# Optimization experiments

Hardware: AMD Instinct MI355X
Metric: run time of the kernel (lower is better)

## Reference

```python
import jax, jax.numpy as jnp
import numpy as np

E = 768   # embed_size
H = 64    # head_embed_size
B = 8
T = 4096  # == ctx_size


def setup_inputs() -> dict:
    key = jax.random.key(0)
    k1, k2, k3, k4 = jax.random.split(key, 4)
    inputs = jax.random.normal(k1, (B, T, E), dtype=jnp.float32)
    # Linear weights stored as (E, H) so projection is x @ W
    scale = 1.0 / np.sqrt(E)
    Wq = jax.random.uniform(k2, (E, H), dtype=jnp.float32, minval=-scale, maxval=scale)
    Wk = jax.random.uniform(k3, (E, H), dtype=jnp.float32, minval=-scale, maxval=scale)
    Wv = jax.random.uniform(k4, (E, H), dtype=jnp.float32, minval=-scale, maxval=scale)
    return {"inputs": inputs, "Wq": Wq, "Wk": Wk, "Wv": Wv}


def reference(inputs, Wq, Wk, Wv):
    Tlen = inputs.shape[1]
    q = inputs @ Wq  # (B,T,H)
    k = inputs @ Wk  # (B,T,H)
    v = inputs @ Wv  # (B,T,H)
    # NOTE: original module does NOT scale by 1/sqrt(H) — faithful reproduction.
    scores = jnp.einsum('bqh,bkh->bqk', q, k)  # (B,T,T)
    causal = jnp.tril(jnp.ones((Tlen, Tlen), dtype=bool))
    scores = jnp.where(causal, scores, -jnp.inf)
    attn = jax.nn.softmax(scores, axis=-1)
    # dropout=0 -> identity
    out = jnp.einsum('bqk,bkh->bqh', attn, v)  # (B,T,H)
    return out
```

## Files before the change

### kernel.cpp

```cpp
#include <hip/hip_runtime.h>
#include <hip/hip_bf16.h>

#define E_DIM 768
#define H_DIM 64
#define B_SZ 8
#define T_SZ 4096
#define BT (B_SZ * T_SZ)

typedef __attribute__((ext_vector_type(8))) short short8;
typedef __attribute__((ext_vector_type(4))) float floatx4;

#define RAWBAR() __asm__ volatile("s_waitcnt lgkmcnt(0)\n\ts_barrier" ::: "memory")

static __device__ __forceinline__ unsigned short bf1(float a) {
    __hip_bfloat16 h = __float2bfloat16(a);
    unsigned short u; __builtin_memcpy(&u, &h, 2); return u;
}
static __device__ __forceinline__ unsigned int pk2(float a, float b) {
    __hip_bfloat162 h = __float22bfloat162_rn(float2{a, b});
    unsigned int u; __builtin_memcpy(&u, &h, 4); return u;
}

__global__ __launch_bounds__(256) void prep_w(
    const float* __restrict__ Wq, const float* __restrict__ Wk,
    const float* __restrict__ Wv, unsigned short* __restrict__ Wt)
{
    __shared__ float Ls[64][65];
    const int nt = blockIdx.x;
    const int kc = blockIdx.y;
    const float* __restrict__ W = (nt == 0) ? Wq : (nt == 1) ? Wk : Wv;
    const float scl = (nt == 0) ? 1.44269504088896f : 1.0f;
    const int t = threadIdx.x;
    const int k0 = kc * 64;

#pragma unroll
    for (int it = 0; it < 16; ++it) {
        const int kk = (t >> 6) + it * 4;
        Ls[kk][t & 63] = W[(size_t)(k0 + kk) * H_DIM + (t & 63)];
    }
    __syncthreads();

#pragma unroll
    for (int it = 0; it < 4; ++it) {
        const int nl = (t >> 4) + it * 16;
        const int kl = (t & 15) * 4;
        unsigned int u[2];
        u[0] = pk2(Ls[kl + 0][nl] * scl, Ls[kl + 1][nl] * scl);
        u[1] = pk2(Ls[kl + 2][nl] * scl, Ls[kl + 3][nl] * scl);
        *(uint2*)(Wt + (size_t)(nt * 64 + nl) * E_DIM + k0 + kl) = *(uint2*)u;
    }
}

__global__ __launch_bounds__(768) void proj_mfma(
    const float* __restrict__ X, const unsigned short* __restrict__ Wt,
    unsigned short* __restrict__ Qb, unsigned short* __restrict__ Kb,
    unsigned short* __restrict__ Vtb)
{
    __shared__ unsigned short Xs[2][16][776];

    const int tid  = threadIdx.x;
    const int wave = tid >> 6, lane = tid & 63;
    const int row  = lane & 15, quad = lane >> 4;
    const int m0   = blockIdx.x * 128;

    short8 bfr[24];
    {
        const unsigned short* wp = Wt + (size_t)(wave * 16 + row) * E_DIM + quad * 8;
#pragma unroll
        for (int ks = 0; ks < 24; ++ks) bfr[ks] = *(const short8*)(wp + ks * 32);
    }

    const int srow = tid & 15;
    const int sc   = tid >> 4;
    const float* __restrict__ xbase = X + (size_t)(m0 + srow) * E_DIM + sc * 16;

    float4 fx[4];
#define LDX(mt)                                                               \
    {                                                                         \
        const float* p = xbase + (size_t)(mt) * 16 * E_DIM;                   \
        fx[0] = *(const float4*)(p);     fx[1] = *(const float4*)(p + 4);     \
        fx[2] = *(const float4*)(p + 8); fx[3] = *(const float4*)(p + 12);    \
    }
#define STX(buf)                                                              \
    {                                                                         \
        unsigned int tmp[8];                                                  \
        tmp[0] = pk2(fx[0].x, fx[0].y); tmp[1] = pk2(fx[0].z, fx[0].w);       \
        tmp[2] = pk2(fx[1].x, fx[1].y); tmp[3] = pk2(fx[1].z, fx[1].w);       \
        tmp[4] = pk2(fx[2].x, fx[2].y); tmp[5] = pk2(fx[2].z, fx[2].w);       \
        tmp[6] = pk2(fx[3].x, fx[3].y); tmp[7] = pk2(fx[3].z, fx[3].w);       \
        *(int4*)&Xs[buf][srow][sc * 16]     = *(int4*)&tmp[0];                \
        *(int4*)&Xs[buf][srow][sc * 16 + 8] = *(int4*)&tmp[4];                \
    }

    LDX(0); STX(0);
    RAWBAR();

    const int g  = wave >> 2;
    const int h  = (wave & 3) * 16 + row;
    unsigned short* __restrict__ OQK = (g == 0) ? Qb : Kb;
    const int bb = m0 >> 12;

    int cur = 0;
    for (int mt = 0; mt < 8; ++mt) {
        if (mt < 7) LDX(mt + 1);

        floatx4 a0 = (floatx4)0.0f, a1 = (floatx4)0.0f;
        floatx4 a2 = (floatx4)0.0f, a3 = (floatx4)0.0f;
#pragma unroll
        for (int ks = 0; ks < 6; ++ks) {
            const short8 f0 = *(const short8*)&Xs[cur][row][(ks * 4 + 0) * 32 + quad * 8];
            const short8 f1 = *(const short8*)&Xs[cur][row][(ks * 4 + 1) * 32 + quad * 8];
            const short8 f2 = *(const short8*)&Xs[cur][row][(ks * 4 + 2) * 32 + quad * 8];
            const short8 f3 = *(const short8*)&Xs[cur][row][(ks * 4 + 3) * 32 + quad * 8];
            a0 = __builtin_amdgcn_mfma_f32_16x16x32_bf16(f0, bfr[ks * 4 + 0], a0, 0, 0, 0);
            a1 = __builtin_amdgcn_mfma_f32_16x16x32_bf16(f1, bfr[ks * 4 + 1], a1, 0, 0, 0);
            a2 = __builtin_amdgcn_mfma_f32_16x16x32_bf16(f2, bfr[ks * 4 + 2], a2, 0, 0, 0);
            a3 = __builtin_amdgcn_mfma_f32_16x16x32_bf16(f3, bfr[ks * 4 + 3], a3, 0, 0, 0);
        }
        floatx4 acc;
#pragma unroll
        for (int r = 0; r < 4; ++r) acc[r] = (a0[r] + a1[r]) + (a2[r] + a3[r]);

        const int mr = m0 + mt * 16 + quad * 4;
        if (g < 2) {
#pragma unroll
            for (int r = 0; r < 4; ++r)
                OQK[(size_t)(mr + r) * H_DIM + h] = bf1(acc[r]);
        } else {
            const int t0 = mr & 4095;
            unsigned int u[2];
            u[0] = pk2(acc[0], acc[1]); u[1] = pk2(acc[2], acc[3]);
            *(uint2*)(Vtb + ((size_t)bb * H_DIM + h) * T_SZ + t0) = *(uint2*)u;
        }

        if (mt < 7) STX(cur ^ 1);
        RAWBAR();
        cur ^= 1;
    }
#undef LDX
#undef STX
}

__global__ __launch_bounds__(256, 3) void attn_mfma(
    const unsigned short* __restrict__ Qb,
    const unsigned short* __restrict__ Kb,
    const unsigned short* __restrict__ Vtb,
    float* __restrict__ Opart, float* __restrict__ lpart,
    float* __restrict__ Out)
{
    __shared__ __align__(16) unsigned short KVb[2][2][64][72];
    __shared__ __align__(16) unsigned short Ps[4][16][40];
    __shared__ float lc[4][16];

    const int lb   = blockIdx.x;
    const int b    = lb & 7;
    const int s    = lb >> 3;
    const bool split = (s < 128);
    const int qq   = split ? (127 - (s >> 1)) : (191 - s);
    const int half = s & 1;
    const int nkt_tot = (qq >> 1) + 1;
    const int hsp  = (nkt_tot + 1) >> 1;
    const int k0t  = (split && half) ? hsp : 0;
    const int k1t  = (split && !half) ? hsp : nkt_tot;
    const int ktd  = nkt_tot - 1;
    const int n    = k1t - k0t;

    const int tid  = threadIdx.x;
    const int wave = tid >> 6, lane = tid & 63;
    const int col  = lane & 15, quad = lane >> 4;
    const int wq   = wave >> 1;
    const int wk   = wave & 1;

    const size_t base = (size_t)b * T_SZ * H_DIM;
    const int q0  = qq * 32;

    short8 qf0, qf1;
    {
        const unsigned short* qp = Qb + base + (size_t)(q0 + wq * 16 + col) * H_DIM + quad * 8;
        qf0 = *(const short8*)(qp);
        qf1 = *(const short8*)(qp + 32);
    }

    floatx4 o[4];
#pragma unroll
    for (int i = 0; i < 4; ++i) o[i] = (floatx4)0.0f;
    float lp[4] = {0.0f, 0.0f, 0.0f, 0.0f};

    const int krow = tid >> 2, kcol = (tid & 3) * 16;
    const unsigned short* __restrict__ Ksrc = Kb + base + (size_t)krow * H_DIM + kcol;
    const unsigned short* __restrict__ Vsrc = Vtb + ((size_t)b * H_DIM + krow) * T_SZ + kcol;

    int4 kr0, kr1, vr0, vr1;
#define LDKV(t)                                                          \
    {                                                                    \
        const unsigned short* kp = Ksrc + (size_t)(t) * 64 * H_DIM;      \
        kr0 = *(const int4*)kp; kr1 = *(const int4*)(kp + 8);            \
        const unsigned short* vp = Vsrc + (t) * 64;                      \
        vr0 = *(const int4*)vp; vr1 = *(const int4*)(vp + 8);            \
    }
#define STKV(bf)                                                         \
    {                                                                    \
        *(int4*)&KVb[bf][0][krow][kcol] = kr0; *(int4*)&KVb[bf][0][krow][kcol + 8] = kr1; \
        *(int4*)&KVb[bf][1][krow][kcol] = vr0; *(int4*)&KVb[bf][1][krow][kcol + 8] = vr1; \
    }

    LDKV(k0t);
    STKV(0);
    if (n > 1) LDKV(k0t + 1);
    RAWBAR();

    int cur = 0;
    for (int i = 0; i < n; ++i) {
        const int kt = k0t + i;

        floatx4 sv[2];
        __builtin_amdgcn_s_setprio(1);
#pragma unroll
        for (int j = 0; j < 2; ++j) {
            const unsigned short* kp = &KVb[cur][0][(wk * 2 + j) * 16 + col][quad * 8];
            floatx4 a = (floatx4)0.0f;
            a = __builtin_amdgcn_mfma_f32_16x16x32_bf16(qf0, *(const short8*)(kp),      a, 0, 0, 0);
            a = __builtin_amdgcn_mfma_f32_16x16x32_bf16(qf1, *(const short8*)(kp + 32), a, 0, 0, 0);
            sv[j] = a;
        }
        __builtin_amdgcn_s_setprio(0);

        if (kt == ktd) {
#pragma unroll
            for (int j = 0; j < 2; ++j) {
                const int keyg = kt * 64 + wk * 32 + j * 16 + col;
#pragma unroll
                for (int r = 0; r < 4; ++r)
                    if (keyg > q0 + wq * 16 + quad * 4 + r) sv[j][r] = -1e30f;
            }
        }

#pragma unroll
        for (int r = 0; r < 4; ++r) {
#pragma unroll
            for (int j = 0; j < 2; ++j) {
                const float pv = exp2f(fminf(sv[j][r], 110.0f));
                lp[r] += pv;
                Ps[wave][quad * 4 + r][j * 16 + col] = bf1(pv);
            }
        }
        __builtin_amdgcn_wave_barrier();

        {
            const short8 pa = *(const short8*)(&Ps[wave][col][quad * 8]);
            __builtin_amdgcn_s_setprio(1);
#pragma unroll
            for (int d = 0; d < 4; ++d) {
                const short8 vb = *(const short8*)(&KVb[cur][1][d * 16 + col][wk * 32 + quad * 8]);
                o[d] = __builtin_amdgcn_mfma_f32_16x16x32_bf16(pa, vb, o[d], 0, 0, 0);
            }
            __builtin_amdgcn_s_setprio(0);
        }

        if (i + 1 < n) {
            STKV(cur ^ 1);
            if (i + 2 < n) LDKV(kt + 2);
        }
        RAWBAR();
        cur ^= 1;
    }

#pragma unroll
    for (int r = 0; r < 4; ++r) {
        float l = lp[r];
#pragma unroll
        for (int off = 1; off < 16; off <<= 1)
            l += __shfl_xor(l, off, 16);
        if (col == 0) lc[wave][quad * 4 + r] = l;
    }
    __syncthreads();

    float* __restrict__ Oc = (float*)&KVb[0][0][0][0];
#pragma unroll
    for (int r = 0; r < 4; ++r)
#pragma unroll
        for (int d = 0; d < 4; ++d)
            Oc[((wave * 16) + quad * 4 + r) * 64 + d * 16 + col] = o[d][r];
    __syncthreads();

    {
        const int orow = tid >> 3;
        const int d0   = (tid & 7) * 8;
        const int rl   = orow & 15;
        const int wb   = (orow >> 4) * 2;
        const float* p0 = &Oc[((wb * 16) + rl) * 64 + d0];
        const float* p1 = &Oc[(((wb + 1) * 16) + rl) * 64 + d0];
        const float lsum = lc[wb][rl] + lc[wb + 1][rl];
        float4 a0 = *(const float4*)(p0);
        float4 a1 = *(const float4*)(p0 + 4);
        const float4 b0 = *(const float4*)(p1);
        const float4 b1 = *(const float4*)(p1 + 4);
        a0.x += b0.x; a0.y += b0.y; a0.z += b0.z; a0.w += b0.w;
        a1.x += b1.x; a1.y += b1.y; a1.z += b1.z; a1.w += b1.w;
        if (!split) {
            const float inv = 1.0f / lsum;
            a0.x *= inv; a0.y *= inv; a0.z *= inv; a0.w *= inv;
            a1.x *= inv; a1.y *= inv; a1.z *= inv; a1.w *= inv;
            float* op = Out + base + (size_t)(q0 + orow) * H_DIM + d0;
            *(float4*)(op)     = a0;
            *(float4*)(op + 4) = a1;
        } else {
            const int pidx = (b * 64 + (qq - 64)) * 2 + half;
            float* op = Opart + ((size_t)pidx * 32 + orow) * 64 + d0;
            *(float4*)(op)     = a0;
            *(float4*)(op + 4) = a1;
            if ((tid & 7) == 0) lpart[pidx * 32 + orow] = lsum;
        }
    }
#undef LDKV
#undef STKV
}

__global__ __launch_bounds__(256) void attn_combine(
    const float* __restrict__ Opart, const float* __restrict__ lpart,
    float* __restrict__ Out)
{
    const int c   = blockIdx.x;
    const int b   = c >> 6;
    const int qi  = c & 63;
    const int qq  = 64 + qi;
    const int tid = threadIdx.x;
    const int orow = tid >> 3;
    const int d0   = (tid & 7) * 8;
    const int p0   = (b * 64 + qi) * 2;

    const float* P0 = Opart + ((size_t)p0 * 32 + orow) * 64 + d0;
    const float* P1 = P0 + 32 * 64;
    const float inv = 1.0f / (lpart[p0 * 32 + orow] + lpart[(p0 + 1) * 32 + orow]);

    float4 a0 = *(const float4*)(P0);
    float4 a1 = *(const float4*)(P0 + 4);
    const float4 b0 = *(const float4*)(P1);
    const float4 b1 = *(const float4*)(P1 + 4);
    a0.x = (a0.x + b0.x) * inv; a0.y = (a0.y + b0.y) * inv;
    a0.z = (a0.z + b0.z) * inv; a0.w = (a0.w + b0.w) * inv;
    a1.x = (a1.x + b1.x) * inv; a1.y = (a1.y + b1.y) * inv;
    a1.z = (a1.z + b1.z) * inv; a1.w = (a1.w + b1.w) * inv;

    float* op = Out + ((size_t)b * T_SZ + qq * 32 + orow) * H_DIM + d0;
    *(float4*)(op)     = a0;
    *(float4*)(op + 4) = a1;
}

extern "C" void kernel_launch(void* const* d_in, const int* in_sizes, int n_in,
                              void* d_out, int out_size, void* d_ws, size_t ws_size,
                              hipStream_t stream) {
    const float* X  = (const float*)d_in[0];
    const float* Wq = (const float*)d_in[1];
    const float* Wk = (const float*)d_in[2];
    const float* Wv = (const float*)d_in[3];

    unsigned short* Wt  = (unsigned short*)d_ws;
    unsigned short* Qb  = Wt + (size_t)192 * E_DIM;
    unsigned short* Kb  = Qb + (size_t)BT * H_DIM;
    unsigned short* Vtb = Kb + (size_t)BT * H_DIM;
    float* Opart = (float*)(Vtb + (size_t)BT * H_DIM);
    float* lpart = Opart + (size_t)1024 * 32 * 64;

    prep_w<<<dim3(3, 12), 256, 0, stream>>>(Wq, Wk, Wv, Wt);
    proj_mfma<<<256, 768, 0, stream>>>(X, Wt, Qb, Kb, Vtb);
    attn_mfma<<<1536, 256, 0, stream>>>(Qb, Kb, Vtb, Opart, lpart, (float*)d_out);
    attn_combine<<<512, 256, 0, stream>>>(Opart, lpart, (float*)d_out);
}
```

Measured before the change: 226.2 us.

## Keep P in registers via transposed QK MFMA, single-buffer K/V LDS

The score MFMA now computes K·Qᵀ by swapping operands. Each lane then holds probabilities in the A-operand layout of the 16x16x16 bf16 MFMA, so P is packed with v_cvt_pk_bf16_f32 and fed straight into the PV product. This removes the per-wave Ps shared-memory staging and its wave barrier, and shrinks the row-sum reduction to two shuffles. K/V shared memory drops from double to single buffering with an extra barrier per tile, and launch bounds rise from 3 to 6 blocks per CU to trade the lost overlap for occupancy. The PV step now issues twice as many smaller-K MFMAs.

```diff
diff --git a/kernel.cpp b/kernel.cpp
--- a/kernel.cpp
+++ b/kernel.cpp
@@ -8,6 +8,7 @@
 #define BT (B_SZ * T_SZ)
 
 typedef __attribute__((ext_vector_type(8))) short short8;
+typedef __attribute__((ext_vector_type(4))) short bf16x4;
 typedef __attribute__((ext_vector_type(4))) float floatx4;
 
 #define RAWBAR() __asm__ volatile("s_waitcnt lgkmcnt(0)\n\ts_barrier" ::: "memory")
@@ -141,15 +142,14 @@
 #undef STX
 }
 
-__global__ __launch_bounds__(256, 3) void attn_mfma(
+__global__ __launch_bounds__(256, 6) void attn_mfma(
     const unsigned short* __restrict__ Qb,
     const unsigned short* __restrict__ Kb,
     const unsigned short* __restrict__ Vtb,
     float* __restrict__ Opart, float* __restrict__ lpart,
     float* __restrict__ Out)
 {
-    __shared__ __align__(16) unsigned short KVb[2][2][64][72];
-    __shared__ __align__(16) unsigned short Ps[4][16][40];
+    __shared__ __align__(16) unsigned short KV[2][64][72];
     __shared__ float lc[4][16];
 
     const int lb   = blockIdx.x;
@@ -184,7 +184,7 @@
     floatx4 o[4];
 #pragma unroll
     for (int i = 0; i < 4; ++i) o[i] = (floatx4)0.0f;
-    float lp[4] = {0.0f, 0.0f, 0.0f, 0.0f};
+    float lp = 0.0f;
 
     const int krow = tid >> 2, kcol = (tid & 3) * 16;
     const unsigned short* __restrict__ Ksrc = Kb + base + (size_t)krow * H_DIM + kcol;
@@ -198,18 +198,17 @@
         const unsigned short* vp = Vsrc + (t) * 64;                      \
         vr0 = *(const int4*)vp; vr1 = *(const int4*)(vp + 8);            \
     }
-#define STKV(bf)                                                         \
+#define STKV()                                                           \
     {                                                                    \
-        *(int4*)&KVb[bf][0][krow][kcol] = kr0; *(int4*)&KVb[bf][0][krow][kcol + 8] = kr1; \
-        *(int4*)&KVb[bf][1][krow][kcol] = vr0; *(int4*)&KVb[bf][1][krow][kcol + 8] = vr1; \
+        *(int4*)&KV[0][krow][kcol] = kr0; *(int4*)&KV[0][krow][kcol + 8] = kr1; \
+        *(int4*)&KV[1][krow][kcol] = vr0; *(int4*)&KV[1][krow][kcol + 8] = vr1; \
     }
 
     LDKV(k0t);
-    STKV(0);
+    STKV();
     if (n > 1) LDKV(k0t + 1);
     RAWBAR();
 
-    int cur = 0;
     for (int i = 0; i < n; ++i) {
         const int kt = k0t + i;
 
@@ -217,65 +216,66 @@
         __builtin_amdgcn_s_setprio(1);
 #pragma unroll
         for (int j = 0; j < 2; ++j) {
-            const unsigned short* kp = &KVb[cur][0][(wk * 2 + j) * 16 + col][quad * 8];
+            const unsigned short* kp = &KV[0][wk * 32 + j * 16 + col][quad * 8];
             floatx4 a = (floatx4)0.0f;
-            a = __builtin_amdgcn_mfma_f32_16x16x32_bf16(qf0, *(const short8*)(kp),      a, 0, 0, 0);
-            a = __builtin_amdgcn_mfma_f32_16x16x32_bf16(qf1, *(const short8*)(kp + 32), a, 0, 0, 0);
+            a = __builtin_amdgcn_mfma_f32_16x16x32_bf16(*(const short8*)(kp),      qf0, a, 0, 0, 0);
+            a = __builtin_amdgcn_mfma_f32_16x16x32_bf16(*(const short8*)(kp + 32), qf1, a, 0, 0, 0);
             sv[j] = a;
         }
         __builtin_amdgcn_s_setprio(0);
 
         if (kt == ktd) {
+            const int qg = q0 + wq * 16 + col;
 #pragma unroll
             for (int j = 0; j < 2; ++j) {
-                const int keyg = kt * 64 + wk * 32 + j * 16 + col;
+                const int kb0 = kt * 64 + wk * 32 + j * 16 + quad * 4;
 #pragma unroll
                 for (int r = 0; r < 4; ++r)
-                    if (keyg > q0 + wq * 16 + quad * 4 + r) sv[j][r] = -1e30f;
+                    if (kb0 + r > qg) sv[j][r] = -1e30f;
             }
         }
 
-#pragma unroll
-        for (int r = 0; r < 4; ++r) {
+        bf16x4 pa[2];
+#pragma unroll
+        for (int j = 0; j < 2; ++j) {
+            float p0 = exp2f(fminf(sv[j][0], 110.0f));
+            float p1 = exp2f(fminf(sv[j][1], 110.0f));
+            float p2 = exp2f(fminf(sv[j][2], 110.0f));
+            float p3 = exp2f(fminf(sv[j][3], 110.0f));
+            lp += (p0 + p1) + (p2 + p3);
+            unsigned int u0, u1;
+            __asm__("v_cvt_pk_bf16_f32 %0, %1, %2" : "=v"(u0) : "v"(p0), "v"(p1));
+            __asm__("v_cvt_pk_bf16_f32 %0, %1, %2" : "=v"(u1) : "v"(p2), "v"(p3));
+            union { unsigned int u[2]; bf16x4 v; } pu;
+            pu.u[0] = u0; pu.u[1] = u1;
+            pa[j] = pu.v;
+        }
+
+        __builtin_amdgcn_s_setprio(1);
+#pragma unroll
+        for (int d = 0; d < 4; ++d) {
 #pragma unroll
             for (int j = 0; j < 2; ++j) {
-                const float pv = exp2f(fminf(sv[j][r], 110.0f));
-                lp[r] += pv;
-                Ps[wave][quad * 4 + r][j * 16 + col] = bf1(pv);
+                const bf16x4 vb = *(const bf16x4*)(&KV[1][d * 16 + col][wk * 32 + j * 16 + quad * 4]);
+                o[d] = __builtin_amdgcn_mfma_f32_16x16x16bf16_1k(pa[j], vb, o[d], 0, 0, 0);
             }
         }
-        __builtin_amdgcn_wave_barrier();
-
-        {
-            const short8 pa = *(const short8*)(&Ps[wave][col][quad * 8]);
-            __builtin_amdgcn_s_setprio(1);
-#pragma unroll
-            for (int d = 0; d < 4; ++d) {
-                const short8 vb = *(const short8*)(&KVb[cur][1][d * 16 + col][wk * 32 + quad * 8]);
-                o[d] = __builtin_amdgcn_mfma_f32_16x16x32_bf16(pa, vb, o[d], 0, 0, 0);
-            }
-            __builtin_amdgcn_s_setprio(0);
-        }
-
+        __builtin_amdgcn_s_setprio(0);
+
+        RAWBAR();
         if (i + 1 < n) {
-            STKV(cur ^ 1);
+            STKV();
             if (i + 2 < n) LDKV(kt + 2);
         }
         RAWBAR();
-        cur ^= 1;
-    }
-
-#pragma unroll
-    for (int r = 0; r < 4; ++r) {
-        float l = lp[r];
-#pragma unroll
-        for (int off = 1; off < 16; off <<= 1)
-            l += __shfl_xor(l, off, 16);
-        if (col == 0) lc[wave][quad * 4 + r] = l;
-    }
+    }
+
+    lp += __shfl_xor(lp, 16);
+    lp += __shfl_xor(lp, 32);
+    if (quad == 0) lc[wave][col] = lp;
     __syncthreads();
 
-    float* __restrict__ Oc = (float*)&KVb[0][0][0][0];
+    float* __restrict__ Oc = (float*)&KV[0][0][0];
 #pragma unroll
     for (int r = 0; r < 4; ++r)
 #pragma unroll
```

New measurement: 220.1 us. 1.03x faster.
